# Kernel tuning notes

Measured on AMD Instinct MI355X. Metric: run time of the kernel, lower is better.

## Reference

```python
import jax, jax.numpy as jnp
import numpy as np

B, DIM, H, W = 4, 64, 256, 256
HEADS = 8
HID = int(DIM * 2.66)  # 170, IEL hidden_features
EPS_LN = 1e-6


def setup_inputs() -> dict:
    key = jax.random.key(0)
    ks = jax.random.split(key, 16)
    r = lambda k, shape, s=0.02: jax.random.normal(k, shape, jnp.float32) * s
    return {
        "x": jax.random.normal(ks[0], (B, DIM, H, W), jnp.float32),
        "y": jax.random.normal(ks[1], (B, DIM, H, W), jnp.float32),
        # shared channels-first LayerNorm params
        "ln_w": jnp.ones((DIM,), jnp.float32),
        "ln_b": jnp.zeros((DIM,), jnp.float32),
        # CAB params (bias=False)
        "temperature": jnp.ones((HEADS, 1, 1), jnp.float32),
        "wq": r(ks[2], (DIM, DIM)),           # 1x1 conv: [out, in]
        "wq_dw": r(ks[3], (DIM, 1, 3, 3)),    # depthwise 3x3
        "wkv": r(ks[4], (2 * DIM, DIM)),
        "wkv_dw": r(ks[5], (2 * DIM, 1, 3, 3)),
        "w_proj": r(ks[6], (DIM, DIM)),
        # IEL params (bias=False)
        "w_in": r(ks[7], (2 * HID, DIM)),
        "w_dw": r(ks[8], (2 * HID, 1, 3, 3)),
        "w_dw1": r(ks[9], (HID, 1, 3, 3)),
        "w_dw2": r(ks[10], (HID, 1, 3, 3)),
        "w_out": r(ks[11], (DIM, HID)),
    }


def conv1x1(x, w):
    # x: [b,c,h,w], w: [o,c]
    return jnp.einsum('oc,bchw->bohw', w, x)


def dwconv3(x, w):
    # depthwise 3x3, SAME padding; w: [C,1,3,3]
    return jax.lax.conv_general_dilated(
        x, w, window_strides=(1, 1), padding='SAME',
        feature_group_count=x.shape[1],
        dimension_numbers=('NCHW', 'OIHW', 'NCHW'))


def layernorm_cf(x, w, b):
    # channels-first LayerNorm: mean/biased-var over channel dim
    u = jnp.mean(x, axis=1, keepdims=True)
    s = jnp.mean((x - u) ** 2, axis=1, keepdims=True)
    xn = (x - u) / jnp.sqrt(s + EPS_LN)
    return w[None, :, None, None] * xn + b[None, :, None, None]


def l2norm(x):
    # torch F.normalize(dim=-1): x / max(||x||, 1e-12)
    n = jnp.sqrt(jnp.sum(x * x, axis=-1, keepdims=True))
    return x / jnp.maximum(n, 1e-12)


def cab(x, y, temperature, wq, wq_dw, wkv, wkv_dw, w_proj):
    b, c, h, w = x.shape
    q = dwconv3(conv1x1(x, wq), wq_dw)
    kv = dwconv3(conv1x1(y, wkv), wkv_dw)
    k, v = kv[:, :c], kv[:, c:]
    ch = c // HEADS  # channels per head
    q = l2norm(q.reshape(b, HEADS, ch, h * w))
    k = l2norm(k.reshape(b, HEADS, ch, h * w))
    v = v.reshape(b, HEADS, ch, h * w)
    attn = jnp.einsum('bhce,bhde->bhcd', q, k) * temperature[None]  # [b,H,ch,ch]
    attn = jax.nn.softmax(attn, axis=-1)
    out = jnp.einsum('bhcd,bhde->bhce', attn, v).reshape(b, c, h, w)
    return conv1x1(out, w_proj)


def iel(x, w_in, w_dw, w_dw1, w_dw2, w_out):
    x = conv1x1(x, w_in)
    d = dwconv3(x, w_dw)
    x1, x2 = d[:, :HID], d[:, HID:]
    x1 = jnp.tanh(dwconv3(x1, w_dw1)) + x1
    x2 = jnp.tanh(dwconv3(x2, w_dw2)) + x2
    return conv1x1(x1 * x2, w_out)


def reference(x, y, ln_w, ln_b, temperature, wq, wq_dw, wkv, wkv_dw, w_proj,
              w_in, w_dw, w_dw1, w_dw2, w_out):
    # I_LCA block forward
    x = x + cab(layernorm_cf(x, ln_w, ln_b), layernorm_cf(y, ln_w, ln_b),
                temperature, wq, wq_dw, wkv, wkv_dw, w_proj)
    x = x + iel(layernorm_cf(x, ln_w, ln_b), w_in, w_dw, w_dw1, w_dw2, w_out)
    return x
```

## Files before the change

### kernel.cpp

```cpp
#include <hip/hip_runtime.h>
#include <hip/hip_bf16.h>

typedef __hip_bfloat16 bf16;
typedef unsigned short u16;
typedef unsigned int u32;
typedef __attribute__((ext_vector_type(8))) unsigned short ushort8;
typedef __attribute__((ext_vector_type(4))) unsigned int uint4_t;
typedef __attribute__((ext_vector_type(8))) short bf16x8;
typedef __attribute__((ext_vector_type(4))) short bf16x4;
typedef __attribute__((ext_vector_type(4))) float f32x4;
typedef __attribute__((ext_vector_type(2))) _Float16 half2_t;

#define PL 65536
#define EPS_LN 1e-6f

#if __has_builtin(__builtin_amdgcn_fdot2)
#define USE_FDOT2 1
#else
#define USE_FDOT2 0
#endif

__device__ __forceinline__ float fast_tanh(float v){
  float e = __expf(2.f*v);
  return 1.f - 2.f/(e+1.f);
}
__device__ __forceinline__ u16 f2bf(float f){
  bf16 h = __float2bfloat16(f);
  return __builtin_bit_cast(u16, h);
}
__device__ __forceinline__ float bf2f(u16 v){
  u32 u = ((u32)v) << 16;
  return __builtin_bit_cast(float, u);
}
__device__ __forceinline__ u16 f2h(float f){
  _Float16 h = (_Float16)f;
  return __builtin_bit_cast(u16, h);
}
__device__ __forceinline__ float h2f(u16 v){
  _Float16 h = __builtin_bit_cast(_Float16, v);
  return (float)h;
}
__device__ __forceinline__ float dot2h(u32 wpair, u32 kpair, float acc){
#if USE_FDOT2
  return __builtin_amdgcn_fdot2(__builtin_bit_cast(half2_t, wpair),
                                __builtin_bit_cast(half2_t, kpair), acc, false);
#else
  float a0 = h2f((u16)(wpair & 0xffff)), a1 = h2f((u16)(wpair >> 16));
  float k0 = h2f((u16)(kpair & 0xffff)), k1 = h2f((u16)(kpair >> 16));
  return acc + a0*k0 + a1*k1;
#endif
}
__device__ __forceinline__ u32 alignhalf(u32 hi, u32 lo){
  return (lo >> 16) | (hi << 16);
}

__global__ void convert_w(const float* __restrict__ wq, const float* __restrict__ wkv,
                          const float* __restrict__ win, const float* __restrict__ wout,
                          const float* __restrict__ wproj,
                          u16* __restrict__ Wq, u16* __restrict__ Wkv,
                          u16* __restrict__ Wp0, u16* __restrict__ Wp1,
                          u16* __restrict__ Wproj, u16* __restrict__ Wh){
  int stride = gridDim.x * 256;
  int gid = blockIdx.x * 256 + threadIdx.x;
  for (int i = gid; i < 64*64;  i += stride) Wq[i]  = f2bf(wq[i]);
  for (int i = gid; i < 128*64; i += stride) Wkv[i] = f2bf(wkv[i]);
  for (int i = gid; i < 176*64; i += stride) {
    int r = i >> 6, c = i & 63;
    Wp0[i] = (r < 85) ? f2bf(win[r*64+c]) : ((r < 170) ? f2bf(win[(85+r)*64+c]) : 0);
    Wp1[i] = (r < 85) ? f2bf(win[(85+r)*64+c]) : ((r < 170) ? f2bf(win[(170+r)*64+c]) : 0);
  }
  for (int i = gid; i < 64*64; i += stride) Wproj[i] = f2bf(wproj[i]);
  for (int i = gid; i < 64*192; i += stride) {
    int o = i / 192, c = i % 192;
    Wh[i] = (c < 170) ? f2bf(wout[o*170 + c]) : 0;
  }
}

__global__ __launch_bounds__(256) void ln_gemm(
    const float* __restrict__ x, const float* __restrict__ lnw,
    const float* __restrict__ lnb, const u16* __restrict__ W,
    u16* __restrict__ out, int MT, int Mvalid, int fmt) {
  int b  = blockIdx.y;
  int p0 = blockIdx.x * 256;
  int tid = threadIdx.x;
  int lane = tid & 63, wv = tid >> 6;
  __shared__ u16 shX[256][72];
  {
    const float* xb = x + ((size_t)b * 64) * PL + p0 + tid;
    float xn[64];
    float mu = 0.f;
    #pragma unroll
    for (int c = 0; c < 64; ++c) { xn[c] = xb[(size_t)c * PL]; mu += xn[c]; }
    mu *= (1.f/64.f);
    float var = 0.f;
    #pragma unroll
    for (int c = 0; c < 64; ++c) { float d = xn[c]-mu; var += d*d; }
    var *= (1.f/64.f);
    float inv = rsqrtf(var + EPS_LN);
    #pragma unroll
    for (int c8 = 0; c8 < 8; ++c8) {
      ushort8 pk;
      #pragma unroll
      for (int j = 0; j < 8; ++j)
        pk[j] = f2bf((xn[c8*8+j]-mu)*inv*lnw[c8*8+j] + lnb[c8*8+j]);
      *reinterpret_cast<ushort8*>(&shX[tid][c8*8]) = pk;
    }
  }
  __syncthreads();
  int col = lane & 15, kg = lane >> 4;
  int n0 = wv * 64;
  bf16x8 bfr[4][2];
  #pragma unroll
  for (int nt = 0; nt < 4; ++nt)
    #pragma unroll
    for (int kh = 0; kh < 2; ++kh)
      bfr[nt][kh] = *reinterpret_cast<const bf16x8*>(&shX[n0 + nt*16 + col][kh*32 + kg*8]);
  for (int mt = 0; mt < MT; ++mt) {
    bf16x8 a0 = *reinterpret_cast<const bf16x8*>(&W[(mt*16+col)*64      + kg*8]);
    bf16x8 a1 = *reinterpret_cast<const bf16x8*>(&W[(mt*16+col)*64 + 32 + kg*8]);
    #pragma unroll
    for (int nt = 0; nt < 4; ++nt) {
      f32x4 acc = {0.f,0.f,0.f,0.f};
      acc = __builtin_amdgcn_mfma_f32_16x16x32_bf16(a0, bfr[nt][0], acc, 0,0,0);
      acc = __builtin_amdgcn_mfma_f32_16x16x32_bf16(a1, bfr[nt][1], acc, 0,0,0);
      int mbase = mt*16 + kg*4;
      #pragma unroll
      for (int r = 0; r < 4; ++r) {
        int ch = mbase + r;
        if (ch < Mvalid)
          out[((size_t)b*Mvalid + ch)*PL + p0 + n0 + nt*16 + col] =
              fmt ? f2h(acc[r]) : f2bf(acc[r]);
      }
    }
  }
}

__global__ __launch_bounds__(256) void dwconv3v(
    const u16* __restrict__ in, const float* __restrict__ w9,
    u16* __restrict__ out, int C) {
  int plane = blockIdx.y;
  int cch = plane % C;
  int y0 = blockIdx.x * 8;
  int tid = threadIdx.x;
  const u16* ip = in + (size_t)plane * PL;
  __shared__ u16 sh[10][272];
  #pragma unroll
  for (int i = 0; i < 2; ++i) {
    int idx = tid + i*256;
    if (idx < 320) {
      int r = idx >> 5, seg = idx & 31;
      int gy = y0 - 1 + r;
      ushort8 v = {0,0,0,0,0,0,0,0};
      if (gy >= 0 && gy < 256)
        v = *reinterpret_cast<const ushort8*>(ip + gy*256 + seg*8);
      *reinterpret_cast<ushort8*>(&sh[r][8 + seg*8]) = v;
    }
  }
  if (tid < 10) { sh[tid][7] = 0; sh[tid][264] = 0; }
  __syncthreads();
  float wk[9];
  #pragma unroll
  for (int i=0;i<9;++i) wk[i] = w9[cch*9+i];
  int lr = tid >> 5, xs = (tid & 31) * 8;
  float row[3][10];
  #pragma unroll
  for (int i = 0; i < 3; ++i) {
    ushort8 m = *reinterpret_cast<const ushort8*>(&sh[lr+i][8+xs]);
    row[i][0] = bf2f(sh[lr+i][7+xs]);
    #pragma unroll
    for (int j=0;j<8;++j) row[i][1+j] = bf2f((u16)m[j]);
    row[i][9] = bf2f(sh[lr+i][16+xs]);
  }
  ushort8 o;
  #pragma unroll
  for (int j = 0; j < 8; ++j) {
    float a = 0.f;
    #pragma unroll
    for (int i=0;i<3;++i)
      #pragma unroll
      for (int k=0;k<3;++k) a += wk[i*3+k]*row[i][j+k];
    o[j] = f2bf(a);
  }
  int gy = y0 + lr;
  *reinterpret_cast<ushort8*>(out + (size_t)plane*PL + gy*256 + xs) = o;
}

__global__ __launch_bounds__(256) void attn_reduce1(
    const bf16* __restrict__ q, const bf16* __restrict__ kv,
    float* __restrict__ part) {
  int bh = blockIdx.y;
  int b = bh >> 3, h = bh & 7;
  int s = blockIdx.x;
  int t = threadIdx.x;
  const bf16* qb = q  + ((size_t)b*64  + h*8) * PL;
  const bf16* kb = kv + ((size_t)b*128 + h*8) * PL;
  float acc[80];
  #pragma unroll
  for (int i=0;i<80;++i) acc[i]=0.f;
  for (int r = 0; r < 4; ++r) {
    int p = s*1024 + r*256 + t;
    float qv[8], kvv[8];
    #pragma unroll
    for (int c=0;c<8;++c) {
      qv[c]=__bfloat162float(qb[(size_t)c*PL+p]);
      kvv[c]=__bfloat162float(kb[(size_t)c*PL+p]);
    }
    #pragma unroll
    for (int c=0;c<8;++c)
      #pragma unroll
      for (int d=0;d<8;++d) acc[c*8+d] += qv[c]*kvv[d];
    #pragma unroll
    for (int c=0;c<8;++c) { acc[64+c] += qv[c]*qv[c]; acc[72+c] += kvv[c]*kvv[c]; }
  }
  __shared__ float lds[4][80];
  int lane = t & 63, wv = t >> 6;
  #pragma unroll
  for (int i=0;i<80;++i) {
    float v = acc[i];
    for (int off=32; off; off>>=1) v += __shfl_down(v, off);
    if (lane==0) lds[wv][i]=v;
  }
  __syncthreads();
  if (t < 80)
    part[((size_t)bh*64 + s)*80 + t] = lds[0][t]+lds[1][t]+lds[2][t]+lds[3][t];
}

__global__ void attn_reduce2(const float* __restrict__ part, float* __restrict__ red) {
  int bh = blockIdx.x; int t = threadIdx.x;
  if (t < 80) {
    float v = 0.f;
    for (int s=0;s<64;++s) v += part[((size_t)bh*64+s)*80+t];
    red[bh*80+t]=v;
  }
}

__global__ void attn_softmax(const float* __restrict__ red, const float* __restrict__ temp,
                             float* __restrict__ attn) {
  int bh = threadIdx.x;
  if (bh >= 32) return;
  int h = bh & 7;
  const float* r = red + bh*80;
  float nq[8], nk[8];
  for (int c=0;c<8;++c) nq[c] = fmaxf(sqrtf(r[64+c]), 1e-12f);
  for (int d=0;d<8;++d) nk[d] = fmaxf(sqrtf(r[72+d]), 1e-12f);
  float tm = temp[h];
  for (int c=0;c<8;++c) {
    float a[8]; float m=-1e30f;
    for (int d=0;d<8;++d){ a[d] = r[c*8+d]/(nq[c]*nk[d]) * tm; m=fmaxf(m,a[d]); }
    float ss=0.f;
    for (int d=0;d<8;++d){ a[d]=__expf(a[d]-m); ss+=a[d]; }
    float inv=1.f/ss;
    for (int d=0;d<8;++d) attn[bh*64 + c*8 + d] = a[d]*inv;
  }
}

__global__ __launch_bounds__(256) void attn_pv(
    const bf16* __restrict__ kv, const float* __restrict__ attnb,
    u16* __restrict__ o_pm) {
  int p = blockIdx.x * 256 + threadIdx.x;
  int b = p >> 16, pix = p & 65535;
  __shared__ float at[512];
  for (int i=threadIdx.x; i<512; i+=256) at[i]=attnb[b*512+i];
  __syncthreads();
  const bf16* vb = kv + ((size_t)b*128 + 64)*PL + pix;
  u16* ob = o_pm + ((size_t)b*PL + pix)*64;
  #pragma unroll
  for (int h=0;h<8;++h){
    float vv[8];
    #pragma unroll
    for (int d=0;d<8;++d) vv[d]=__bfloat162float(vb[(size_t)(h*8+d)*PL]);
    ushort8 pk;
    #pragma unroll
    for (int c=0;c<8;++c){
      float acc=0.f;
      #pragma unroll
      for (int d=0;d<8;++d) acc += at[h*64+c*8+d]*vv[d];
      pk[c] = f2bf(acc);
    }
    *reinterpret_cast<ushort8*>(ob + h*8) = pk;
  }
}

__global__ __launch_bounds__(256) void gemm_proj(
    const u16* __restrict__ Wp, const u16* __restrict__ o_pm,
    const float* __restrict__ x, float* __restrict__ out) {
  int b  = blockIdx.y;
  int p0 = blockIdx.x * 256;
  int tid = threadIdx.x;
  int lane = tid & 63, wv = tid >> 6;
  __shared__ u16 shX[256][72];
  const u16* src = o_pm + ((size_t)b * PL + p0) * 64;
  #pragma unroll
  for (int c8 = 0; c8 < 8; ++c8)
    *reinterpret_cast<ushort8*>(&shX[tid][c8*8]) =
        *reinterpret_cast<const ushort8*>(src + (size_t)tid*64 + c8*8);
  __syncthreads();
  int col = lane & 15, kg = lane >> 4;
  int n0 = wv * 64;
  bf16x8 bfr[4][2];
  #pragma unroll
  for (int nt = 0; nt < 4; ++nt)
    #pragma unroll
    for (int kh = 0; kh < 2; ++kh)
      bfr[nt][kh] = *reinterpret_cast<const bf16x8*>(&shX[n0 + nt*16 + col][kh*32 + kg*8]);
  #pragma unroll
  for (int mt = 0; mt < 4; ++mt) {
    bf16x8 a0 = *reinterpret_cast<const bf16x8*>(&Wp[(mt*16+col)*64      + kg*8]);
    bf16x8 a1 = *reinterpret_cast<const bf16x8*>(&Wp[(mt*16+col)*64 + 32 + kg*8]);
    #pragma unroll
    for (int nt = 0; nt < 4; ++nt) {
      f32x4 acc = {0.f,0.f,0.f,0.f};
      acc = __builtin_amdgcn_mfma_f32_16x16x32_bf16(a0, bfr[nt][0], acc, 0,0,0);
      acc = __builtin_amdgcn_mfma_f32_16x16x32_bf16(a1, bfr[nt][1], acc, 0,0,0);
      #pragma unroll
      for (int r = 0; r < 4; ++r) {
        int o = mt*16 + kg*4 + r;
        size_t idx = ((size_t)(b*64 + o))*PL + p0 + n0 + nt*16 + col;
        out[idx] = x[idx] + acc[r];
      }
    }
  }
}

__global__ __launch_bounds__(256) void iel_gate2(
    const u16* __restrict__ t, const float* __restrict__ wdw,
    const float* __restrict__ wdw1, const float* __restrict__ wdw2,
    u16* __restrict__ P, int hcbase) {
  int pj = blockIdx.y;
  int b = pj / 85, j = pj % 85;
  int hc = hcbase + j;
  int bx = blockIdx.x;
  int y0 = (bx >> 2) * 32;
  int x0 = (bx & 3) * 64;
  int tid = threadIdx.x;

  __shared__ u16 sT[2][36][88];
  __shared__ u16 sD[2][34][88];

  const u16* t1 = t + (size_t)(b*170 + j) * PL;
  const u16* t2 = t + (size_t)(b*170 + 85 + j) * PL;

  #pragma unroll
  for (int it = 0; it < 3; ++it) {
    int idx = tid + it*256;
    if (idx < 720) {
      int pl = idx / 360, rem = idx % 360;
      int r = rem / 10, ch = rem % 10;
      int gy = y0 + r - 2;
      int gxb = x0 - 8 + ch*8;
      ushort8 v = {0,0,0,0,0,0,0,0};
      if (gy >= 0 && gy < 256 && gxb >= 0 && gxb <= 248)
        v = *reinterpret_cast<const ushort8*>((pl ? t2 : t1) + gy*256 + gxb);
      *reinterpret_cast<ushort8*>(&sT[pl][r][ch*8]) = v;
    }
  }
  __syncthreads();

  #pragma unroll
  for (int it = 0; it < 3; ++it) {
    int idx = tid + it*256;
    if (idx < 612) {
      int pl = idx / 306, rem = idx % 306;
      int r = rem / 9, si = rem % 9;
      int gy = y0 + r - 1;
      const float* kp = wdw + (pl ? (170+hc) : hc)*9;
      u32 k01[3], k2z[3];
      #pragma unroll
      for (int i=0;i<3;++i){
        k01[i] = (u32)f2h(kp[i*3+0]) | ((u32)f2h(kp[i*3+1]) << 16);
        k2z[i] = (u32)f2h(kp[i*3+2]);
      }
      float a[8];
      #pragma unroll
      for (int jj=0;jj<8;++jj) a[jj]=0.f;
      #pragma unroll
      for (int i = 0; i < 3; ++i) {
        ushort8 A0 = *reinterpret_cast<const ushort8*>(&sT[pl][r+i][si*8]);
        ushort8 A1 = *reinterpret_cast<const ushort8*>(&sT[pl][r+i][si*8+8]);
        uint4_t wa = __builtin_bit_cast(uint4_t, A0);
        uint4_t wb = __builtin_bit_cast(uint4_t, A1);
        u32 R1=wa.y, R2=wa.z, R3=wa.w, R4=wb.x, R5=wb.y, R6=wb.z;
        u32 prs[10] = { alignhalf(R2,R1), R2, alignhalf(R3,R2), R3,
                        alignhalf(R4,R3), R4, alignhalf(R5,R4), R5,
                        alignhalf(R6,R5), R6 };
        #pragma unroll
        for (int jj = 0; jj < 8; ++jj)
          a[jj] = dot2h(prs[jj+2], k2z[i], dot2h(prs[jj], k01[i], a[jj]));
      }
      int gx0 = x0 + si*8 - 4;
      bool rowok = (gy >= 0 && gy < 256);
      ushort8 dv;
      #pragma unroll
      for (int jj = 0; jj < 8; ++jj) {
        int gx = gx0 + jj;
        bool ok = rowok && gx >= 0 && gx < 256;
        dv[jj] = ok ? f2h(a[jj]) : (u16)0;
      }
      *reinterpret_cast<ushort8*>(&sD[pl][r][si*8]) = dv;
    }
  }
  __syncthreads();

  int ry = tid >> 3, seg = tid & 7;
  float x1[8], x2[8];
  #pragma unroll
  for (int pl = 0; pl < 2; ++pl) {
    const float* kp = (pl ? wdw2 : wdw1) + hc*9;
    u32 k01[3], k2z[3];
    #pragma unroll
    for (int i=0;i<3;++i){
      k01[i] = (u32)f2h(kp[i*3+0]) | ((u32)f2h(kp[i*3+1]) << 16);
      k2z[i] = (u32)f2h(kp[i*3+2]);
    }
    float a[8];
    #pragma unroll
    for (int jj=0;jj<8;++jj) a[jj]=0.f;
    float dc[8];
    #pragma unroll
    for (int i = 0; i < 3; ++i) {
      ushort8 A0 = *reinterpret_cast<const ushort8*>(&sD[pl][ry+i][seg*8]);
      ushort8 A1 = *reinterpret_cast<const ushort8*>(&sD[pl][ry+i][seg*8+8]);
      uint4_t wa = __builtin_bit_cast(uint4_t, A0);
      uint4_t wb = __builtin_bit_cast(uint4_t, A1);
      u32 R1=wa.y, R2=wa.z, R3=wa.w, R4=wb.x, R5=wb.y, R6=wb.z;
      u32 prs[10] = { alignhalf(R2,R1), R2, alignhalf(R3,R2), R3,
                      alignhalf(R4,R3), R4, alignhalf(R5,R4), R5,
                      alignhalf(R6,R5), R6 };
      #pragma unroll
      for (int jj = 0; jj < 8; ++jj)
        a[jj] = dot2h(prs[jj+2], k2z[i], dot2h(prs[jj], k01[i], a[jj]));
      if (i == 1) {
        u32 cw[4] = { wa.z, wa.w, wb.x, wb.y };
        #pragma unroll
        for (int jj = 0; jj < 8; ++jj) {
          u32 wrd = cw[(jj+4)/2 - 2];
          u16 hv = (jj & 1) ? (u16)(wrd >> 16) : (u16)(wrd & 0xffff);
          dc[jj] = h2f(hv);
        }
      }
    }
    #pragma unroll
    for (int jj = 0; jj < 8; ++jj) {
      float g = fast_tanh(a[jj]) + dc[jj];
      if (pl) x2[jj] = g; else x1[jj] = g;
    }
  }
  ushort8 o;
  #pragma unroll
  for (int jj = 0; jj < 8; ++jj) o[jj] = f2bf(x1[jj]*x2[jj]);
  int gy = y0 + ry;
  *reinterpret_cast<ushort8*>(
      P + ((size_t)(b*170 + hcbase + j))*PL + gy*256 + x0 + seg*8) = o;
}

__global__ __launch_bounds__(256) void iel_gemm(
    const u16* __restrict__ Wh, const u16* __restrict__ P,
    float* __restrict__ out) {
  int b  = blockIdx.y;
  int p0 = blockIdx.x * 256;
  int tid = threadIdx.x;
  int lane = tid & 63, wv = tid >> 6;
  int col = lane & 15, kg = lane >> 4;
  int n0 = wv * 64;
  __shared__ u16 shP[256][36];
  f32x4 acc[4][4];
  #pragma unroll
  for (int mt=0;mt<4;++mt)
    #pragma unroll
    for (int nt=0;nt<4;++nt) acc[mt][nt] = (f32x4){0.f,0.f,0.f,0.f};

  int kk = tid & 31, q = tid >> 5;
  for (int c = 0; c < 6; ++c) {
    int hcl = c*32 + kk;
    ushort8 v[4];
    if (hcl < 170) {
      const u16* src = P + (size_t)(b*170 + hcl)*PL + p0 + q*32;
      #pragma unroll
      for (int jj=0;jj<4;++jj) v[jj] = *reinterpret_cast<const ushort8*>(src + jj*8);
    } else {
      #pragma unroll
      for (int jj=0;jj<4;++jj) v[jj] = (ushort8){0,0,0,0,0,0,0,0};
    }
    __syncthreads();
    #pragma unroll
    for (int jj=0;jj<4;++jj)
      #pragma unroll
      for (int i=0;i<8;++i) shP[q*32 + jj*8 + i][kk] = v[jj][i];
    __syncthreads();
    #pragma unroll
    for (int nt = 0; nt < 4; ++nt) {
      int px = n0 + nt*16 + col;
      const bf16x4* pp = reinterpret_cast<const bf16x4*>(&shP[px][kg*8]);
      bf16x4 plo = pp[0], phi = pp[1];
      bf16x8 bfrag;
      #pragma unroll
      for (int jj=0;jj<4;++jj){ bfrag[jj]=plo[jj]; bfrag[4+jj]=phi[jj]; }
      #pragma unroll
      for (int mt = 0; mt < 4; ++mt) {
        bf16x8 a = *reinterpret_cast<const bf16x8*>(&Wh[(mt*16+col)*192 + c*32 + kg*8]);
        acc[mt][nt] = __builtin_amdgcn_mfma_f32_16x16x32_bf16(a, bfrag, acc[mt][nt], 0,0,0);
      }
    }
  }
  #pragma unroll
  for (int mt=0; mt<4; ++mt)
    #pragma unroll
    for (int nt=0; nt<4; ++nt)
      #pragma unroll
      for (int r=0; r<4; ++r){
        int o = mt*16 + kg*4 + r;
        size_t idx = ((size_t)(b*64 + o))*PL + p0 + n0 + nt*16 + col;
        out[idx] += acc[mt][nt][r];
      }
}

extern "C" void kernel_launch(void* const* d_in, const int* in_sizes, int n_in,
                              void* d_out, int out_size, void* d_ws, size_t ws_size,
                              hipStream_t stream) {
  const float* x      = (const float*)d_in[0];
  const float* y      = (const float*)d_in[1];
  const float* lnw    = (const float*)d_in[2];
  const float* lnb    = (const float*)d_in[3];
  const float* temp   = (const float*)d_in[4];
  const float* wq     = (const float*)d_in[5];
  const float* wq_dw  = (const float*)d_in[6];
  const float* wkv    = (const float*)d_in[7];
  const float* wkv_dw = (const float*)d_in[8];
  const float* wproj  = (const float*)d_in[9];
  const float* w_in   = (const float*)d_in[10];
  const float* w_dw   = (const float*)d_in[11];
  const float* w_dw1  = (const float*)d_in[12];
  const float* w_dw2  = (const float*)d_in[13];
  const float* w_out  = (const float*)d_in[14];

  char* base = (char*)d_ws;
  u16* Wq_b    = (u16*)(base + 0);
  u16* Wkv_b   = (u16*)(base + 8192);
  u16* Wp0     = (u16*)(base + 24576);
  u16* Wp1     = (u16*)(base + 47104);
  u16* Wproj_b = (u16*)(base + 69632);
  u16* Wh      = (u16*)(base + 77824);
  char* A = base + 131072;

  u16*  kvpre = (u16*)A;
  u16*  kvd   = (u16*)(A + 89128960);
  u16*  qpre  = (u16*)A;
  u16*  qd    = (u16*)(A + 33554432);
  float* part = (float*)A;
  float* red  = (float*)(A + 1048576);
  float* attnb= (float*)(A + 1572864);
  u16*  o_pm  = (u16*)(A + 4194304);
  u16*  tbuf  = (u16*)A;
  u16*  Pbuf  = (u16*)(A + 89128960);
  float* xmid = (float*)d_out;

  convert_w<<<64, 256, 0, stream>>>(wq, wkv, w_in, w_out, wproj,
                                    Wq_b, Wkv_b, Wp0, Wp1, Wproj_b, Wh);

  ln_gemm<<<dim3(256,4), 256, 0, stream>>>(y, lnw, lnb, Wkv_b, kvpre, 8, 128, 0);
  dwconv3v<<<dim3(32,512), 256, 0, stream>>>(kvpre, wkv_dw, kvd, 128);
  ln_gemm<<<dim3(256,4), 256, 0, stream>>>(x, lnw, lnb, Wq_b, qpre, 4, 64, 0);
  dwconv3v<<<dim3(32,256), 256, 0, stream>>>(qpre, wq_dw, qd, 64);
  attn_reduce1<<<dim3(64,32), 256, 0, stream>>>((const bf16*)qd, (const bf16*)kvd, part);
  attn_reduce2<<<32, 128, 0, stream>>>(part, red);
  attn_softmax<<<1, 64, 0, stream>>>(red, temp, attnb);
  attn_pv<<<1024, 256, 0, stream>>>((const bf16*)kvd, attnb, o_pm);
  gemm_proj<<<dim3(256,4), 256, 0, stream>>>(Wproj_b, o_pm, x, xmid);

  ln_gemm<<<dim3(256,4), 256, 0, stream>>>(xmid, lnw, lnb, Wp0, tbuf, 11, 170, 1);
  iel_gate2<<<dim3(32,340), 256, 0, stream>>>(tbuf, w_dw, w_dw1, w_dw2, Pbuf, 0);
  ln_gemm<<<dim3(256,4), 256, 0, stream>>>(xmid, lnw, lnb, Wp1, tbuf, 11, 170, 1);
  iel_gate2<<<dim3(32,340), 256, 0, stream>>>(tbuf, w_dw, w_dw1, w_dw2, Pbuf, 85);
  iel_gemm<<<dim3(256,4), 256, 0, stream>>>(Wh, Pbuf, xmid);
}
```

Before: 506.0 us.

## Fuse attention PV into projection GEMM and vectorize attention reduction loads

Merges the attn_pv kernel into the projection GEMM, so the P·V output is written straight into shared memory and the o_pm intermediate never makes a round trip through global memory. The attention reduction now loads 8 contiguous bf16 per thread as vectors, with half as many blocks and partial sums, which cuts scalar load instructions. The iel_gate2 shared-memory tiles are also shrunk in padding to lower LDS use, which could change bank-conflict behaviour.

```diff
diff --git a/kernel.cpp b/kernel.cpp
--- a/kernel.cpp
+++ b/kernel.cpp
@@ -192,25 +192,29 @@
   int b = bh >> 3, h = bh & 7;
   int s = blockIdx.x;
   int t = threadIdx.x;
-  const bf16* qb = q  + ((size_t)b*64  + h*8) * PL;
-  const bf16* kb = kv + ((size_t)b*128 + h*8) * PL;
+  int p = s*2048 + t*8;
+  const u16* qb = reinterpret_cast<const u16*>(q)  + ((size_t)b*64  + h*8) * PL + p;
+  const u16* kb = reinterpret_cast<const u16*>(kv) + ((size_t)b*128 + h*8) * PL + p;
+  ushort8 vq[8], vk[8];
+  #pragma unroll
+  for (int c=0;c<8;++c) {
+    vq[c] = *reinterpret_cast<const ushort8*>(qb + (size_t)c*PL);
+    vk[c] = *reinterpret_cast<const ushort8*>(kb + (size_t)c*PL);
+  }
   float acc[80];
   #pragma unroll
   for (int i=0;i<80;++i) acc[i]=0.f;
-  for (int r = 0; r < 4; ++r) {
-    int p = s*1024 + r*256 + t;
-    float qv[8], kvv[8];
-    #pragma unroll
-    for (int c=0;c<8;++c) {
-      qv[c]=__bfloat162float(qb[(size_t)c*PL+p]);
-      kvv[c]=__bfloat162float(kb[(size_t)c*PL+p]);
-    }
+  #pragma unroll
+  for (int e = 0; e < 8; ++e) {
+    float qe[8], ke[8];
+    #pragma unroll
+    for (int c=0;c<8;++c) { qe[c]=bf2f((u16)vq[c][e]); ke[c]=bf2f((u16)vk[c][e]); }
     #pragma unroll
     for (int c=0;c<8;++c)
       #pragma unroll
-      for (int d=0;d<8;++d) acc[c*8+d] += qv[c]*kvv[d];
-    #pragma unroll
-    for (int c=0;c<8;++c) { acc[64+c] += qv[c]*qv[c]; acc[72+c] += kvv[c]*kvv[c]; }
+      for (int d=0;d<8;++d) acc[c*8+d] += qe[c]*ke[d];
+    #pragma unroll
+    for (int c=0;c<8;++c) { acc[64+c] += qe[c]*qe[c]; acc[72+c] += ke[c]*ke[c]; }
   }
   __shared__ float lds[4][80];
   int lane = t & 63, wv = t >> 6;
@@ -222,14 +226,14 @@
   }
   __syncthreads();
   if (t < 80)
-    part[((size_t)bh*64 + s)*80 + t] = lds[0][t]+lds[1][t]+lds[2][t]+lds[3][t];
+    part[((size_t)bh*32 + s)*80 + t] = lds[0][t]+lds[1][t]+lds[2][t]+lds[3][t];
 }
 
 __global__ void attn_reduce2(const float* __restrict__ part, float* __restrict__ red) {
   int bh = blockIdx.x; int t = threadIdx.x;
   if (t < 80) {
     float v = 0.f;
-    for (int s=0;s<64;++s) v += part[((size_t)bh*64+s)*80+t];
+    for (int s=0;s<32;++s) v += part[((size_t)bh*32+s)*80+t];
     red[bh*80+t]=v;
   }
 }
@@ -254,46 +258,37 @@
   }
 }
 
-__global__ __launch_bounds__(256) void attn_pv(
+__global__ __launch_bounds__(256) void attn_pv_proj(
     const bf16* __restrict__ kv, const float* __restrict__ attnb,
-    u16* __restrict__ o_pm) {
-  int p = blockIdx.x * 256 + threadIdx.x;
-  int b = p >> 16, pix = p & 65535;
-  __shared__ float at[512];
-  for (int i=threadIdx.x; i<512; i+=256) at[i]=attnb[b*512+i];
-  __syncthreads();
-  const bf16* vb = kv + ((size_t)b*128 + 64)*PL + pix;
-  u16* ob = o_pm + ((size_t)b*PL + pix)*64;
-  #pragma unroll
-  for (int h=0;h<8;++h){
-    float vv[8];
-    #pragma unroll
-    for (int d=0;d<8;++d) vv[d]=__bfloat162float(vb[(size_t)(h*8+d)*PL]);
-    ushort8 pk;
-    #pragma unroll
-    for (int c=0;c<8;++c){
-      float acc=0.f;
-      #pragma unroll
-      for (int d=0;d<8;++d) acc += at[h*64+c*8+d]*vv[d];
-      pk[c] = f2bf(acc);
-    }
-    *reinterpret_cast<ushort8*>(ob + h*8) = pk;
-  }
-}
-
-__global__ __launch_bounds__(256) void gemm_proj(
-    const u16* __restrict__ Wp, const u16* __restrict__ o_pm,
-    const float* __restrict__ x, float* __restrict__ out) {
+    const u16* __restrict__ Wp, const float* __restrict__ x,
+    float* __restrict__ out) {
   int b  = blockIdx.y;
   int p0 = blockIdx.x * 256;
   int tid = threadIdx.x;
   int lane = tid & 63, wv = tid >> 6;
+  __shared__ float at[512];
   __shared__ u16 shX[256][72];
-  const u16* src = o_pm + ((size_t)b * PL + p0) * 64;
-  #pragma unroll
-  for (int c8 = 0; c8 < 8; ++c8)
-    *reinterpret_cast<ushort8*>(&shX[tid][c8*8]) =
-        *reinterpret_cast<const ushort8*>(src + (size_t)tid*64 + c8*8);
+  for (int i=tid; i<512; i+=256) at[i]=attnb[b*512+i];
+  __syncthreads();
+  {
+    int pix = p0 + tid;
+    const bf16* vb = kv + ((size_t)b*128 + 64)*PL + pix;
+    #pragma unroll
+    for (int h=0;h<8;++h){
+      float vv[8];
+      #pragma unroll
+      for (int d=0;d<8;++d) vv[d]=__bfloat162float(vb[(size_t)(h*8+d)*PL]);
+      ushort8 pk;
+      #pragma unroll
+      for (int c=0;c<8;++c){
+        float acc=0.f;
+        #pragma unroll
+        for (int d=0;d<8;++d) acc += at[h*64+c*8+d]*vv[d];
+        pk[c] = f2bf(acc);
+      }
+      *reinterpret_cast<ushort8*>(&shX[tid][h*8]) = pk;
+    }
+  }
   __syncthreads();
   int col = lane & 15, kg = lane >> 4;
   int n0 = wv * 64;
@@ -334,8 +329,8 @@
   int x0 = (bx & 3) * 64;
   int tid = threadIdx.x;
 
-  __shared__ u16 sT[2][36][88];
-  __shared__ u16 sD[2][34][88];
+  __shared__ u16 sT[2][36][80];
+  __shared__ u16 sD[2][34][72];
 
   const u16* t1 = t + (size_t)(b*170 + j) * PL;
   const u16* t2 = t + (size_t)(b*170 + 85 + j) * PL;
@@ -549,7 +544,6 @@
   float* part = (float*)A;
   float* red  = (float*)(A + 1048576);
   float* attnb= (float*)(A + 1572864);
-  u16*  o_pm  = (u16*)(A + 4194304);
   u16*  tbuf  = (u16*)A;
   u16*  Pbuf  = (u16*)(A + 89128960);
   float* xmid = (float*)d_out;
@@ -561,11 +555,10 @@
   dwconv3v<<<dim3(32,512), 256, 0, stream>>>(kvpre, wkv_dw, kvd, 128);
   ln_gemm<<<dim3(256,4), 256, 0, stream>>>(x, lnw, lnb, Wq_b, qpre, 4, 64, 0);
   dwconv3v<<<dim3(32,256), 256, 0, stream>>>(qpre, wq_dw, qd, 64);
-  attn_reduce1<<<dim3(64,32), 256, 0, stream>>>((const bf16*)qd, (const bf16*)kvd, part);
+  attn_reduce1<<<dim3(32,32), 256, 0, stream>>>((const bf16*)qd, (const bf16*)kvd, part);
   attn_reduce2<<<32, 128, 0, stream>>>(part, red);
   attn_softmax<<<1, 64, 0, stream>>>(red, temp, attnb);
-  attn_pv<<<1024, 256, 0, stream>>>((const bf16*)kvd, attnb, o_pm);
-  gemm_proj<<<dim3(256,4), 256, 0, stream>>>(Wproj_b, o_pm, x, xmid);
+  attn_pv_proj<<<dim3(256,4), 256, 0, stream>>>((const bf16*)kvd, attnb, Wproj_b, x, xmid);
 
   ln_gemm<<<dim3(256,4), 256, 0, stream>>>(xmid, lnw, lnb, Wp0, tbuf, 11, 170, 1);
   iel_gate2<<<dim3(32,340), 256, 0, stream>>>(tbuf, w_dw, w_dw1, w_dw2, Pbuf, 0);
```

After: 462.9 us. 8.5% less time.
